# Kernel optimization log

Measured on AMD Instinct MI355X. Metric: run time of the kernel, lower is better.

Reference implementation:

```python
import jax, jax.numpy as jnp
from jax import lax
import numpy as np

V = 30000   # vocab_size
E = 64      # embedding_dim
H = 64      # lstm_units
K = 9       # num_tags
B = 512
T = 512


def setup_inputs() -> dict:
    key = jax.random.key(0)
    ks = jax.random.split(key, 12)
    s = 0.05
    return {
        "tokens": jax.random.randint(ks[0], (B, T), 0, V),
        "emb":   jax.random.normal(ks[1], (V + 1, E), dtype=jnp.float32) * s,
        "Wf": jax.random.normal(ks[2], (E, 4 * H), dtype=jnp.float32) * s,
        "Uf": jax.random.normal(ks[3], (H, 4 * H), dtype=jnp.float32) * s,
        "bf": jnp.zeros((4 * H,), dtype=jnp.float32),
        "Wb": jax.random.normal(ks[4], (E, 4 * H), dtype=jnp.float32) * s,
        "Ub": jax.random.normal(ks[5], (H, 4 * H), dtype=jnp.float32) * s,
        "bb": jnp.zeros((4 * H,), dtype=jnp.float32),
        "Wd": jax.random.normal(ks[6], (2 * H, K), dtype=jnp.float32) * s,
        "bd": jnp.zeros((K,), dtype=jnp.float32),
        "trans": jax.random.normal(ks[7], (K, K), dtype=jnp.float32) * s,
    }


def _lstm(x_tm, mask_tm, W, U, b):
    """Keras-convention LSTM over time-major x_tm [T,B,E]; masked steps carry state."""
    Bsz = x_tm.shape[1]
    h0 = jnp.zeros((Bsz, U.shape[0]), x_tm.dtype)
    c0 = jnp.zeros_like(h0)

    def step(carry, inp):
        h, c = carry
        xt, mt = inp                      # xt [B,E], mt [B] bool
        z = xt @ W + h @ U + b            # [B,4H], gate order i,f,g,o
        i, f, g, o = jnp.split(z, 4, axis=-1)
        c_new = jax.nn.sigmoid(f) * c + jax.nn.sigmoid(i) * jnp.tanh(g)
        h_new = jax.nn.sigmoid(o) * jnp.tanh(c_new)
        m = mt[:, None]
        h2 = jnp.where(m, h_new, h)
        c2 = jnp.where(m, c_new, c)
        return (h2, c2), h2

    _, hs = lax.scan(step, (h0, c0), (x_tm, mask_tm))
    return hs                              # [T,B,H]


def _viterbi(pot, mask, trans):
    """Batched Viterbi decode. pot [B,T,K], mask [B,T] bool, trans [K,K]."""
    pot_t = pot.transpose(1, 0, 2)         # [T,B,K]
    m_t = mask.T                           # [T,B]
    alpha0 = pot_t[0]
    ident = jnp.arange(K, dtype=jnp.int32)[None, :]

    def step(alpha, inp):
        p, m = inp                         # p [B,K], m [B]
        scores = alpha[:, :, None] + trans[None]   # [B, prev K, next K]
        best = scores.max(axis=1)
        bp = scores.argmax(axis=1).astype(jnp.int32)
        mm = m[:, None]
        alpha_new = jnp.where(mm, best + p, alpha)
        bp = jnp.where(mm, bp, ident)
        return alpha_new, bp

    alpha, bps = lax.scan(step, alpha0, (pot_t[1:], m_t[1:]))   # bps [T-1,B,K]
    last = alpha.argmax(axis=-1).astype(jnp.int32)              # [B]

    def back(tag, bp):
        prev = jnp.take_along_axis(bp, tag[:, None], axis=1)[:, 0]
        return prev, prev

    _, ys = lax.scan(back, last, bps, reverse=True)             # ys[t] = tag_t, t<T-1
    tags = jnp.concatenate([ys, last[None]], axis=0).T          # [B,T]
    return jnp.where(mask, tags, 0)


def reference(tokens, emb, Wf, Uf, bf, Wb, Ub, bb, Wd, bd, trans):
    mask = tokens != 0                     # mask_zero semantics
    x = emb[tokens]                        # [B,T,E]
    x_tm = x.transpose(1, 0, 2)            # [T,B,E]
    m_tm = mask.T
    hf = _lstm(x_tm, m_tm, Wf, Uf, bf)                     # forward dir
    hb = _lstm(x_tm[::-1], m_tm[::-1], Wb, Ub, bb)[::-1]   # backward dir
    h = jnp.concatenate([hf, hb], axis=-1).transpose(1, 0, 2)  # [B,T,2H]
    potentials = h @ Wd + bd               # CRF emission potentials [B,T,K]
    decoded = _viterbi(potentials, mask, trans)
    seq_len = mask.sum(axis=1).astype(jnp.int32)
    return decoded, potentials, seq_len
```

## Files before the change

kernel.cpp:

```cpp
#include <hip/hip_runtime.h>

#define BB 512
#define TT 512
#define KK 9
#define VP1 30001
#define BTK ((size_t)BB * TT * KK)

typedef __attribute__((ext_vector_type(8))) short short8;
typedef __attribute__((ext_vector_type(4))) float float4v;

__device__ __forceinline__ float sigm(float x) {
    return __builtin_amdgcn_rcpf(1.0f + __expf(-x));
}
__device__ __forceinline__ float tanh_(float x) {
    return 1.0f - 2.0f * __builtin_amdgcn_rcpf(__expf(2.0f * x) + 1.0f);
}

__device__ __forceinline__ unsigned short f2bf(float f) {
    unsigned int u = __float_as_uint(f);
    unsigned int r = u + 0x7fffu + ((u >> 16) & 1u);
    return (unsigned short)(r >> 16);
}
__device__ __forceinline__ float bflo2f(unsigned int d) { return __uint_as_float(d << 16); }
__device__ __forceinline__ float bfhi2f(unsigned int d) { return __uint_as_float(d & 0xffff0000u); }

__device__ __forceinline__ float bcast(float v, int i) {
    return __uint_as_float(__builtin_amdgcn_readlane(__float_as_uint(v), i));
}

__device__ __forceinline__ void block_sync_lds() {
    __builtin_amdgcn_s_waitcnt(0xC07F);
    __builtin_amdgcn_s_barrier();
}

__global__ __launch_bounds__(256)
void wswz_kernel(const float* __restrict__ Wf, const float* __restrict__ bfv,
                 const float* __restrict__ Wb, const float* __restrict__ bbv,
                 unsigned short* __restrict__ wswz, float* __restrict__ bsw)
{
    const int tid = threadIdx.x;
#pragma unroll
    for (int it = 0; it < 16; ++it) {
        int o = blockIdx.x * 4096 + it * 256 + tid;
        int k = o & 63, c = o >> 6;
        int dir = c >> 8, rem = c & 255;
        int u = rem >> 2, g = rem & 3;
        float val = (dir ? Wb : Wf)[k * 256 + g * 64 + u];
        wswz[o] = f2bf(val);
    }
    if (blockIdx.x == 0) {
#pragma unroll
        for (int h = 0; h < 2; ++h) {
            int c = h * 256 + tid;
            int dir = c >> 8, rem = c & 255;
            bsw[c] = (dir ? bbv : bfv)[(rem & 3) * 64 + (rem >> 2)];
        }
    }
}

__global__ __launch_bounds__(256, 1)
void embw_kernel(const float* __restrict__ emb,
                 const unsigned short* __restrict__ wswz, const float* __restrict__ bsw,
                 unsigned short* __restrict__ embw)
{
    const int v0 = blockIdx.x * 64;
    const int tid = threadIdx.x;
    const int w = tid >> 6, lane = tid & 63;
    const int l16 = lane & 15, quad = lane >> 4;

    __shared__ __align__(16) unsigned short clds[64][520];

    short8 bFr[8][2];
    float biasn[8];
#pragma unroll
    for (int n = 0; n < 8; ++n) {
        int c = w * 128 + n * 16 + l16;
        biasn[n] = bsw[c];
        const unsigned short* wp = wswz + c * 64;
#pragma unroll
        for (int q = 0; q < 2; ++q)
            bFr[n][q] = *(const short8*)(wp + q * 32 + quad * 8);
    }

    short8 aFr[4][2];
#pragma unroll
    for (int mt = 0; mt < 4; ++mt) {
        int vrow = v0 + mt * 16 + l16;
        if (vrow >= VP1) vrow = VP1 - 1;
        const float* er = emb + (size_t)vrow * 64;
#pragma unroll
        for (int q = 0; q < 2; ++q) {
            const float* p = er + q * 32 + quad * 8;
            float4 x0 = *(const float4*)(p);
            float4 x1 = *(const float4*)(p + 4);
            short8 v;
            v[0] = (short)f2bf(x0.x); v[1] = (short)f2bf(x0.y);
            v[2] = (short)f2bf(x0.z); v[3] = (short)f2bf(x0.w);
            v[4] = (short)f2bf(x1.x); v[5] = (short)f2bf(x1.y);
            v[6] = (short)f2bf(x1.z); v[7] = (short)f2bf(x1.w);
            aFr[mt][q] = v;
        }
    }

    float4v acc[4][8];
#pragma unroll
    for (int mt = 0; mt < 4; ++mt)
#pragma unroll
        for (int n = 0; n < 8; ++n) {
            acc[mt][n][0] = biasn[n]; acc[mt][n][1] = biasn[n];
            acc[mt][n][2] = biasn[n]; acc[mt][n][3] = biasn[n];
        }
#pragma unroll
    for (int mt = 0; mt < 4; ++mt)
#pragma unroll
        for (int n = 0; n < 8; ++n) {
            acc[mt][n] = __builtin_amdgcn_mfma_f32_16x16x32_bf16(aFr[mt][0], bFr[n][0], acc[mt][n], 0, 0, 0);
            acc[mt][n] = __builtin_amdgcn_mfma_f32_16x16x32_bf16(aFr[mt][1], bFr[n][1], acc[mt][n], 0, 0, 0);
        }

#pragma unroll
    for (int mt = 0; mt < 4; ++mt)
#pragma unroll
        for (int n = 0; n < 8; ++n) {
            int cc = w * 128 + n * 16 + l16;
#pragma unroll
            for (int r = 0; r < 4; ++r)
                clds[mt * 16 + quad * 4 + r][cc] = f2bf(acc[mt][n][r]);
        }
    __syncthreads();

#pragma unroll
    for (int it = 0; it < 16; ++it) {
        int idx = it * 256 + tid;
        int row = idx >> 6, chunk = idx & 63;
        if (v0 + row < VP1) {
            uint4 val = *(const uint4*)&clds[row][chunk * 8];
            *(uint4*)(embw + (size_t)(v0 + row) * 512 + chunk * 8) = val;
        }
    }
}

__global__ __launch_bounds__(320, 1)
void rec_kernel(const int* __restrict__ tokens,
                const unsigned short* __restrict__ embw,
                const float* __restrict__ Uf, const float* __restrict__ Ub,
                const float* __restrict__ Wd,
                float* __restrict__ potf, float* __restrict__ potb)
{
    const int blk = blockIdx.x;
    const int dir = blk >> 7;
    const int row0 = (blk & 127) * 4;
    const int tid = threadIdx.x;
    const int wv = tid >> 6;
    const int lane = tid & 63;
    const int l16 = lane & 15, quad = lane >> 4;

    const float* Up = dir ? Ub : Uf;
    float* pot = dir ? potb : potf;

    __shared__ int tokl[4][TT + 8];
    __shared__ __align__(16) unsigned short hl[2][16][72];

    for (int i = tid; i < 2 * 16 * 72; i += 320)
        ((unsigned short*)hl)[i] = 0;
    for (int i = tid; i < 4 * TT; i += 320) {
        int r = i >> 9, t = i & 511;
        tokl[r][t] = tokens[(row0 + r) * TT + t];
    }

    if (wv < 4) {
        const int w = wv;
        const int u = w * 16 + l16;

        short8 bU[4][2];
#pragma unroll
        for (int g = 0; g < 4; ++g)
#pragma unroll
            for (int q = 0; q < 2; ++q) {
                short8 v;
#pragma unroll
                for (int j = 0; j < 8; ++j) {
                    int k = q * 32 + quad * 8 + j;
                    v[j] = (short)f2bf(Up[k * 256 + g * 64 + u]);
                }
                bU[g][q] = v;
            }

        __syncthreads();

        int tokA[4], tokB[4];
        const uint2* ebase = (const uint2*)embw + dir * 64 + u;
#pragma unroll
        for (int d = 0; d < 4; ++d) {
            int td = dir ? (TT - 1 - d) : d;
            int td4 = dir ? (TT - 1 - (d + 4)) : (d + 4);
            tokA[d] = tokl[quad][td];
            tokB[d] = tokl[quad][td4];
        }
        uint2 zxp[4];
#pragma unroll
        for (int d = 0; d < 4; ++d)
            zxp[d] = ebase[(size_t)tokA[d] << 7];

        float c_st = 0.f, h_st = 0.f;
        float4v accA[4], accB[4];
        const float4v zz = {0.f, 0.f, 0.f, 0.f};
#pragma unroll
        for (int g = 0; g < 4; ++g) { accA[g] = zz; accB[g] = zz; }

        for (int sb = 0; sb < TT; sb += 4) {
#pragma unroll
            for (int ss = 0; ss < 4; ++ss) {
                const int s = sb + ss;
                const int tcur = tokA[ss];
                const uint2 zcur = zxp[ss];

                hl[ss & 1][quad * 4][u] = f2bf(h_st);

                if (s + 4 < TT)
                    zxp[ss] = ebase[(size_t)tokB[ss] << 7];
                tokA[ss] = tokB[ss];

                block_sync_lds();

                const unsigned short* hrow = &hl[ss & 1][l16][0];
                short8 a0 = *(const short8*)(hrow + quad * 8);
                short8 a1 = *(const short8*)(hrow + 32 + quad * 8);

                if (s + 8 < TT) {
                    int t8 = dir ? (TT - 1 - (s + 8)) : (s + 8);
                    tokB[ss] = tokl[quad][t8];
                }

                accA[0][0] = bflo2f(zcur.x);
                accA[1][0] = bfhi2f(zcur.x);
                accA[2][0] = bflo2f(zcur.y);
                accA[3][0] = bfhi2f(zcur.y);

                accA[2] = __builtin_amdgcn_mfma_f32_16x16x32_bf16(a0, bU[2][0], accA[2], 0, 0, 0);
                accB[2] = __builtin_amdgcn_mfma_f32_16x16x32_bf16(a1, bU[2][1], zz, 0, 0, 0);
                accA[0] = __builtin_amdgcn_mfma_f32_16x16x32_bf16(a0, bU[0][0], accA[0], 0, 0, 0);
                accB[0] = __builtin_amdgcn_mfma_f32_16x16x32_bf16(a1, bU[0][1], zz, 0, 0, 0);
                accA[1] = __builtin_amdgcn_mfma_f32_16x16x32_bf16(a0, bU[1][0], accA[1], 0, 0, 0);
                accB[1] = __builtin_amdgcn_mfma_f32_16x16x32_bf16(a1, bU[1][1], zz, 0, 0, 0);
                accA[3] = __builtin_amdgcn_mfma_f32_16x16x32_bf16(a0, bU[3][0], accA[3], 0, 0, 0);
                accB[3] = __builtin_amdgcn_mfma_f32_16x16x32_bf16(a1, bU[3][1], zz, 0, 0, 0);

                {
                    float zg_ = accA[2][0] + accB[2][0];
                    float tg  = tanh_(zg_);
                    float zi_ = accA[0][0] + accB[0][0];
                    float si  = sigm(zi_);
                    float zf_ = accA[1][0] + accB[1][0];
                    float zo_ = accA[3][0] + accB[3][0];
                    float cn  = sigm(zf_) * c_st + si * tg;
                    float hn  = sigm(zo_) * tanh_(cn);
                    bool m = (tcur != 0);
                    h_st = m ? hn : h_st;
                    c_st = m ? cn : c_st;
                }
            }
        }

        hl[0][quad * 4][u] = f2bf(h_st);
        block_sync_lds();
    } else {
        short8 bW[2];
#pragma unroll
        for (int q = 0; q < 2; ++q) {
            short8 v;
#pragma unroll
            for (int j = 0; j < 8; ++j) {
                int k = q * 32 + quad * 8 + j;
                v[j] = (l16 < KK) ? (short)f2bf(Wd[(dir * 64 + k) * KK + l16]) : (short)0;
            }
            bW[q] = v;
        }

        __syncthreads();

        int vOff = ((row0 + quad) * TT + (dir ? (TT - 1) : 0)) * KK + l16;
        const int vStep = dir ? -KK : KK;
        const bool potAct = (l16 < KK);
        const float4v zz = {0.f, 0.f, 0.f, 0.f};

        for (int s = 0; s <= TT; ++s) {
            block_sync_lds();
            const unsigned short* hrow = &hl[s & 1][l16][0];
            short8 a0 = *(const short8*)(hrow + quad * 8);
            short8 a1 = *(const short8*)(hrow + 32 + quad * 8);
            if (s > 0) {
                float4v accP;
                accP = __builtin_amdgcn_mfma_f32_16x16x32_bf16(a0, bW[0], zz, 0, 0, 0);
                accP = __builtin_amdgcn_mfma_f32_16x16x32_bf16(a1, bW[1], accP, 0, 0, 0);
                if (potAct) pot[vOff] = accP[0];
                vOff += vStep;
            }
        }
    }
}

__global__ __launch_bounds__(128)
void viterbi_kernel(const int* __restrict__ tokens,
                    const float* __restrict__ potf, const float* __restrict__ potb,
                    const float* __restrict__ bd, const float* __restrict__ trans,
                    float* __restrict__ dec_out, float* __restrict__ pot_out,
                    float* __restrict__ seq_out)
{
    const int row = blockIdx.x;
    const int L = threadIdx.x;
    const int wave = L >> 6;
    const int lane = L & 63;

    __shared__ float pl[TT * KK + 16];
    __shared__ unsigned char bpl[(TT - 1) * KK];
    __shared__ unsigned char maskl[TT + 8];
    __shared__ unsigned char segmap[64][KK];
    __shared__ unsigned char bseq[65];
    __shared__ float decl_[TT];
    __shared__ float bdl[16];

    if (L < KK) bdl[L] = bd[L];
    if (L < 8) maskl[TT + L] = 0;
    pl[TT * KK + (L & 15)] = 0.f;

    if (wave == 0) {
        int cnt = 0;
#pragma unroll
        for (int ch = 0; ch < TT / 64; ++ch) {
            int tk = tokens[row * TT + ch * 64 + lane];
            int m = (tk != 0) ? 1 : 0;
            maskl[ch * 64 + lane] = (unsigned char)m;
            cnt += m;
        }
        for (int off = 32; off > 0; off >>= 1) cnt += __shfl_down(cnt, off);
        if (lane == 0) seq_out[row] = (float)cnt;
    }
    __syncthreads();

    const size_t base = (size_t)row * (TT * KK);
    {
        int r9 = L % KK;
        for (int i = L; i < TT * KK; i += 128) {
            float s = potf[base + i] + potb[base + i] + bdl[r9];
            pl[i] = s;
            pot_out[base + i] = s;
            r9 += 2;
            if (r9 >= KK) r9 -= KK;
        }
    }
    __syncthreads();

    int last = 0;
    if (wave == 0) {
        float treg[KK];
#pragma unroll
        for (int i = 0; i < KK; ++i) treg[i] = (lane < KK) ? trans[i * KK + lane] : 0.f;

        float alpha = (lane < KK) ? pl[lane] : -1e30f;
        float pnext = (lane < KK) ? pl[KK + lane] : 0.f;
        int mnext = maskl[1];
#pragma unroll 4
        for (int t = 1; t < TT; ++t) {
            float p = pnext;
            int m = mnext;
            pnext = (lane < KK) ? pl[(t + 1) * KK + lane] : 0.f;
            mnext = maskl[t + 1];

            float sc[KK];
#pragma unroll
            for (int i = 0; i < KK; ++i) sc[i] = bcast(alpha, i) + treg[i];
            float b0 = fmaxf(fmaxf(fmaxf(sc[0], sc[1]), sc[2]),
                       fmaxf(fmaxf(fmaxf(sc[3], sc[4]), sc[5]),
                             fmaxf(fmaxf(sc[6], sc[7]), sc[8])));
            int i0 = 8;
#pragma unroll
            for (int i = 7; i >= 0; --i) i0 = (sc[i] == b0) ? i : i0;

            alpha = m ? (b0 + p) : alpha;
            int bpv = m ? i0 : lane;
            if (lane < KK) bpl[(t - 1) * KK + lane] = (unsigned char)bpv;
        }
        float sc[KK];
#pragma unroll
        for (int i = 0; i < KK; ++i) sc[i] = bcast(alpha, i);
        float b0 = fmaxf(fmaxf(fmaxf(sc[0], sc[1]), sc[2]),
                   fmaxf(fmaxf(fmaxf(sc[3], sc[4]), sc[5]),
                         fmaxf(fmaxf(sc[6], sc[7]), sc[8])));
        last = 8;
#pragma unroll
        for (int i = 7; i >= 0; --i) last = (sc[i] == b0) ? i : last;
    }
    __syncthreads();

    if (wave == 0) {
        int l = lane;
#pragma unroll
        for (int x = 0; x < KK; ++x) {
            int y = x;
#pragma unroll
            for (int d = 7; d >= 0; --d) {
                int t = 8 * l + d;
                if (t < TT - 1) y = bpl[t * KK + y];
            }
            segmap[l][x] = (unsigned char)y;
        }
    }
    __syncthreads();
    if (L == 0) {
        int cur = last;
        bseq[64] = (unsigned char)last;
        for (int l = 63; l >= 0; --l) {
            cur = segmap[l][cur];
            bseq[l] = (unsigned char)cur;
        }
    }
    __syncthreads();
    if (wave == 0) {
        int l = lane;
        int cur = bseq[l + 1];
#pragma unroll
        for (int d = 7; d >= 0; --d) {
            int t = 8 * l + d;
            if (t < TT - 1) cur = bpl[t * KK + cur];
            decl_[t] = (maskl[t] != 0) ? (float)cur : 0.f;
        }
    }
    __syncthreads();
    for (int i = L; i < TT; i += 128)
        dec_out[(size_t)row * TT + i] = decl_[i];
}

extern "C" void kernel_launch(void* const* d_in, const int* in_sizes, int n_in,
                              void* d_out, int out_size, void* d_ws, size_t ws_size,
                              hipStream_t stream)
{
    const int*   tokens = (const int*)d_in[0];
    const float* emb    = (const float*)d_in[1];
    const float* Wf     = (const float*)d_in[2];
    const float* Uf     = (const float*)d_in[3];
    const float* bfv    = (const float*)d_in[4];
    const float* Wb     = (const float*)d_in[5];
    const float* Ub     = (const float*)d_in[6];
    const float* bbv    = (const float*)d_in[7];
    const float* Wd     = (const float*)d_in[8];
    const float* bd     = (const float*)d_in[9];
    const float* trans  = (const float*)d_in[10];

    float* out     = (float*)d_out;
    float* dec_out = out;
    float* pot_out = out + (size_t)BB * TT;
    float* seq_out = out + (size_t)BB * TT + BTK;

    float* potf = (float*)d_ws;
    float* potb = potf + BTK;
    unsigned short* embw = (unsigned short*)(potb + BTK);
    unsigned short* wswz = (unsigned short*)potf;
    float* bsw = (float*)((char*)potf + 512 * 64 * sizeof(unsigned short));

    hipLaunchKernelGGL(wswz_kernel, dim3(8), dim3(256), 0, stream,
                       Wf, bfv, Wb, bbv, wswz, bsw);
    hipLaunchKernelGGL(embw_kernel, dim3(469), dim3(256), 0, stream,
                       emb, wswz, bsw, embw);
    hipLaunchKernelGGL(rec_kernel, dim3(256), dim3(320), 0, stream,
                       tokens, embw, Uf, Ub, Wd, potf, potb);
    hipLaunchKernelGGL(viterbi_kernel, dim3(BB), dim3(128), 0, stream,
                       tokens, potf, potb, bd, trans, dec_out, pot_out, seq_out);
}
```

Before: 372.2 us.

## Streamline recurrent step token prefetch and use packed bf16 conversion

```diff
diff --git a/kernel.cpp b/kernel.cpp
--- a/kernel.cpp
+++ b/kernel.cpp
@@ -8,6 +8,8 @@
 
 typedef __attribute__((ext_vector_type(8))) short short8;
 typedef __attribute__((ext_vector_type(4))) float float4v;
+typedef __attribute__((ext_vector_type(4))) int int4v;
+typedef __attribute__((ext_vector_type(4))) unsigned int uint4v;
 
 __device__ __forceinline__ float sigm(float x) {
     return __builtin_amdgcn_rcpf(1.0f + __expf(-x));
@@ -23,6 +25,12 @@
 }
 __device__ __forceinline__ float bflo2f(unsigned int d) { return __uint_as_float(d << 16); }
 __device__ __forceinline__ float bfhi2f(unsigned int d) { return __uint_as_float(d & 0xffff0000u); }
+
+__device__ __forceinline__ unsigned int cvtpk_bf16(float a, float b) {
+    unsigned int r;
+    asm("v_cvt_pk_bf16_f32 %0, %1, %2" : "=v"(r) : "v"(a), "v"(b));
+    return r;
+}
 
 __device__ __forceinline__ float bcast(float v, int i) {
     return __uint_as_float(__builtin_amdgcn_readlane(__float_as_uint(v), i));
@@ -93,12 +101,12 @@
             const float* p = er + q * 32 + quad * 8;
             float4 x0 = *(const float4*)(p);
             float4 x1 = *(const float4*)(p + 4);
-            short8 v;
-            v[0] = (short)f2bf(x0.x); v[1] = (short)f2bf(x0.y);
-            v[2] = (short)f2bf(x0.z); v[3] = (short)f2bf(x0.w);
-            v[4] = (short)f2bf(x1.x); v[5] = (short)f2bf(x1.y);
-            v[6] = (short)f2bf(x1.z); v[7] = (short)f2bf(x1.w);
-            aFr[mt][q] = v;
+            uint4v pk;
+            pk[0] = cvtpk_bf16(x0.x, x0.y);
+            pk[1] = cvtpk_bf16(x0.z, x0.w);
+            pk[2] = cvtpk_bf16(x1.x, x1.y);
+            pk[3] = cvtpk_bf16(x1.z, x1.w);
+            aFr[mt][q] = __builtin_bit_cast(short8, pk);
         }
     }
 
@@ -158,15 +166,16 @@
     const float* Up = dir ? Ub : Uf;
     float* pot = dir ? potb : potf;
 
-    __shared__ int tokl[4][TT + 8];
+    __shared__ __align__(16) int tokl[4][TT + 8];
     __shared__ __align__(16) unsigned short hl[2][16][72];
 
     for (int i = tid; i < 2 * 16 * 72; i += 320)
         ((unsigned short*)hl)[i] = 0;
     for (int i = tid; i < 4 * TT; i += 320) {
         int r = i >> 9, t = i & 511;
-        tokl[r][t] = tokens[(row0 + r) * TT + t];
-    }
+        tokl[r][t] = tokens[(row0 + r) * TT + (dir ? (TT - 1 - t) : t)];
+    }
+    if (tid < 32) tokl[tid >> 3][TT + (tid & 7)] = 0;
 
     if (wv < 4) {
         const int w = wv;
@@ -187,20 +196,15 @@
             }
 
         __syncthreads();
-
-        int tokA[4], tokB[4];
+        __builtin_amdgcn_s_setprio(1);
+
         const uint2* ebase = (const uint2*)embw + dir * 64 + u;
-#pragma unroll
-        for (int d = 0; d < 4; ++d) {
-            int td = dir ? (TT - 1 - d) : d;
-            int td4 = dir ? (TT - 1 - (d + 4)) : (d + 4);
-            tokA[d] = tokl[quad][td];
-            tokB[d] = tokl[quad][td4];
-        }
+
+        int4v tca = *(const int4v*)&tokl[quad][0];
         uint2 zxp[4];
 #pragma unroll
         for (int d = 0; d < 4; ++d)
-            zxp[d] = ebase[(size_t)tokA[d] << 7];
+            zxp[d] = ebase[(size_t)tca[d] << 7];
 
         float c_st = 0.f, h_st = 0.f;
         float4v accA[4], accB[4];
@@ -209,33 +213,24 @@
         for (int g = 0; g < 4; ++g) { accA[g] = zz; accB[g] = zz; }
 
         for (int sb = 0; sb < TT; sb += 4) {
+            int4v tnx = *(const int4v*)&tokl[quad][sb + 4];
 #pragma unroll
             for (int ss = 0; ss < 4; ++ss) {
-                const int s = sb + ss;
-                const int tcur = tokA[ss];
+                const int tcur = tca[ss];
                 const uint2 zcur = zxp[ss];
 
-                hl[ss & 1][quad * 4][u] = f2bf(h_st);
-
-                if (s + 4 < TT)
-                    zxp[ss] = ebase[(size_t)tokB[ss] << 7];
-                tokA[ss] = tokB[ss];
-
-                block_sync_lds();
-
-                const unsigned short* hrow = &hl[ss & 1][l16][0];
-                short8 a0 = *(const short8*)(hrow + quad * 8);
-                short8 a1 = *(const short8*)(hrow + 32 + quad * 8);
-
-                if (s + 8 < TT) {
-                    int t8 = dir ? (TT - 1 - (s + 8)) : (s + 8);
-                    tokB[ss] = tokl[quad][t8];
-                }
+                hl[ss & 1][quad * 4][u] = (unsigned short)cvtpk_bf16(h_st, h_st);
 
                 accA[0][0] = bflo2f(zcur.x);
                 accA[1][0] = bfhi2f(zcur.x);
                 accA[2][0] = bflo2f(zcur.y);
                 accA[3][0] = bfhi2f(zcur.y);
+
+                block_sync_lds();
+
+                const unsigned short* hrow = &hl[ss & 1][l16][0];
+                short8 a0 = *(const short8*)(hrow + quad * 8);
+                short8 a1 = *(const short8*)(hrow + 32 + quad * 8);
 
                 accA[2] = __builtin_amdgcn_mfma_f32_16x16x32_bf16(a0, bU[2][0], accA[2], 0, 0, 0);
                 accB[2] = __builtin_amdgcn_mfma_f32_16x16x32_bf16(a1, bU[2][1], zz, 0, 0, 0);
@@ -245,6 +240,8 @@
                 accB[1] = __builtin_amdgcn_mfma_f32_16x16x32_bf16(a1, bU[1][1], zz, 0, 0, 0);
                 accA[3] = __builtin_amdgcn_mfma_f32_16x16x32_bf16(a0, bU[3][0], accA[3], 0, 0, 0);
                 accB[3] = __builtin_amdgcn_mfma_f32_16x16x32_bf16(a1, bU[3][1], zz, 0, 0, 0);
+
+                zxp[ss] = ebase[(size_t)tnx[ss] << 7];
 
                 {
                     float zg_ = accA[2][0] + accB[2][0];
@@ -260,9 +257,11 @@
                     c_st = m ? cn : c_st;
                 }
             }
-        }
-
-        hl[0][quad * 4][u] = f2bf(h_st);
+            tca = tnx;
+        }
+        __builtin_amdgcn_s_setprio(0);
+
+        hl[0][quad * 4][u] = (unsigned short)cvtpk_bf16(h_st, h_st);
         block_sync_lds();
     } else {
         short8 bW[2];
```

Result: faster. 341.4 us (-8.3%).
